# Performance work log

Hardware: AMD Instinct MI355X
Metric: run time of the kernel (lower is better)

## Reference

```python
import jax, jax.numpy as jnp
import numpy as np

K = 3
LAMBDA_AMP = 0.1
N_NODES = 100000
N_EDGES = 1600000
D_FEAT = 50


def _proximal_l21(x, lambda_):
    # rowwise L2,1 shrinkage: scale each row by max(||row||-lambda,0)/||row||
    row_norm = jnp.linalg.norm(x, axis=1)  # [N]
    score = jnp.maximum(row_norm - lambda_, 0.0)
    score = jnp.where(row_norm > 0, score / jnp.where(row_norm > 0, row_norm, 1.0), score)
    return score[:, None] * x


def setup_inputs() -> dict:
    key = jax.random.key(0)
    k1, k2, k3, k4 = jax.random.split(key, 4)
    feat = jax.random.normal(k1, (N_NODES, D_FEAT), dtype=jnp.float32)
    edge_weight = jax.random.uniform(k2, (N_EDGES,), dtype=jnp.float32)
    src = jax.random.randint(k3, (N_EDGES,), 0, N_NODES, dtype=jnp.int32)
    dst = jax.random.randint(k4, (N_EDGES,), 0, N_NODES, dtype=jnp.int32)
    return {"feat": feat, "edge_weight": edge_weight, "src": src, "dst": dst}


def reference(feat, edge_weight, src, dst):
    n = feat.shape[0]
    # add self-loops (add_self_loop=True), self-loop weight = 1
    loop = jnp.arange(n, dtype=src.dtype)
    src_f = jnp.concatenate([src, loop])
    dst_f = jnp.concatenate([dst, loop])
    ew = jnp.concatenate([edge_weight, jnp.ones((n,), dtype=edge_weight.dtype)])

    # norm='both': w_ji = ew / (sqrt(out_deg(j)) * sqrt(in_deg(i))), weighted degrees
    out_deg = jax.ops.segment_sum(ew, src_f, num_segments=n)
    in_deg = jax.ops.segment_sum(ew, dst_f, num_segments=n)
    inv_sqrt_out = jnp.where(out_deg > 0, out_deg, 1.0) ** -0.5 * (out_deg > 0)
    inv_sqrt_in = jnp.where(in_deg > 0, in_deg, 1.0) ** -0.5 * (in_deg > 0)
    w = ew * inv_sqrt_out[src_f] * inv_sqrt_in[dst_f]  # [E+N]

    lam = LAMBDA_AMP
    gamma = 1.0 / (2.0 * (1.0 - lam))
    hh = feat
    x = feat
    for _ in range(K):
        # compute_LX: x - A_norm x  (u_mul_e + sum == SpMM over edges)
        agg = jax.ops.segment_sum(x[src_f] * w[:, None], dst_f, num_segments=n)
        lx = x - agg
        y = x - gamma * 2.0 * (1.0 - lam) * lx
        x = hh + _proximal_l21(y - hh, gamma * lam)
    return x
```

## Files before the change

### kernel.cpp

```cpp
#include <hip/hip_runtime.h>
#include <hip/hip_bf16.h>
#include <hip/hip_fp16.h>

#define D 50
#define PADH 64
#define GLAM 0.05555555555555555f
#define SCAN_B 1024
#define FIXS 8388608.0f
#define INV_FIXS (1.0f / 8388608.0f)
#define WSC 32768.0f
#define INV_WSC (1.0f / 32768.0f)
#define EPB 4096
#define EPT 8
#define B2T 512
#define BSH 9
#define BMSK 511u
#define BT 512
#define MAXB 256
#define MAXRUN 12288
#define NXCD 8

typedef unsigned long long u64;

__global__ void k_b1p(const int* __restrict__ src, const int* __restrict__ dst,
                      int* __restrict__ mat, const float* __restrict__ feat,
                      __half* __restrict__ xp, int e, int nblk, int nbuk, int n) {
    if ((int)blockIdx.x < nblk) {
        __shared__ unsigned hd[MAXB], hs[MAXB];
        for (int j = threadIdx.x; j < nbuk; j += blockDim.x) { hd[j] = 0; hs[j] = 0; }
        __syncthreads();
        int base = blockIdx.x * EPB;
        int end = base + EPB; if (end > e) end = e;
        for (int i = base + threadIdx.x; i < end; i += blockDim.x) {
            int t = __builtin_nontemporal_load(dst + i);
            int s = __builtin_nontemporal_load(src + i);
            atomicAdd(&hd[t >> BSH], 1u);
            atomicAdd(&hs[s >> BSH], 1u);
        }
        __syncthreads();
        for (int j = threadIdx.x; j < nbuk; j += blockDim.x) {
            mat[j * nblk + blockIdx.x] = (int)hd[j];
            mat[(nbuk + j) * nblk + blockIdx.x] = (int)hs[j];
        }
    } else {
        int i = ((int)blockIdx.x - nblk) * (int)blockDim.x + (int)threadIdx.x;
        if (i < n * PADH) {
            int node = i >> 6, col = i & 63;
            xp[i] = (col < D) ? __float2half_rn(feat[node * D + col]) : __half(0.0f);
        }
    }
}

__global__ void k_scan1(const int* __restrict__ cnt, int* __restrict__ out,
                        int* __restrict__ bsum, int n) {
    __shared__ int s[SCAN_B];
    int i = blockIdx.x * SCAN_B + threadIdx.x;
    int v = (i < n) ? cnt[i] : 0;
    s[threadIdx.x] = v; __syncthreads();
    for (int off = 1; off < SCAN_B; off <<= 1) {
        int t = (threadIdx.x >= (unsigned)off) ? s[threadIdx.x - off] : 0;
        __syncthreads();
        s[threadIdx.x] += t; __syncthreads();
    }
    if (i < n) out[i] = s[threadIdx.x] - v;
    if (threadIdx.x == SCAN_B - 1) bsum[blockIdx.x] = s[threadIdx.x];
}

__global__ void k_scan2(int* __restrict__ bsum, int nb) {
    __shared__ int s[SCAN_B];
    int v = (threadIdx.x < (unsigned)nb) ? bsum[threadIdx.x] : 0;
    s[threadIdx.x] = v; __syncthreads();
    for (int off = 1; off < SCAN_B; off <<= 1) {
        int t = (threadIdx.x >= (unsigned)off) ? s[threadIdx.x - off] : 0;
        __syncthreads();
        s[threadIdx.x] += t; __syncthreads();
    }
    if (threadIdx.x < (unsigned)nb) bsum[threadIdx.x] = s[threadIdx.x] - v;
}

__global__ void k_scan3(int* __restrict__ out, const int* __restrict__ bsum, int n) {
    int i = blockIdx.x * SCAN_B + threadIdx.x;
    if (i < n) out[i] += bsum[blockIdx.x];
}

__device__ __forceinline__ int xcd_swz(int p, int nwg) {
    int q = nwg / NXCD, r = nwg % NXCD;
    int xcd = p % NXCD, idx = p / NXCD;
    return (xcd < r ? xcd * (q + 1) : r * (q + 1) + (xcd - r) * q) + idx;
}

__global__ __launch_bounds__(B2T, 4) void k_b2(
                     const float* __restrict__ ew, const int* __restrict__ src,
                     const int* __restrict__ dst, const int* __restrict__ msc,
                     u64* __restrict__ bind, unsigned* __restrict__ bins,
                     int e, int nblk, int nbuk) {
    __shared__ unsigned cd[MAXB], cs[MAXB];
    __shared__ unsigned ld[MAXB], ls[MAXB];
    __shared__ int gbd[MAXB], gbs[MAXB];
    __shared__ u64 sd[EPB];
    __shared__ unsigned ss[EPB];
    __shared__ unsigned char bdd[EPB], bds[EPB];
    int tid = threadIdx.x;
    int wb = xcd_swz((int)blockIdx.x, nblk);
    if (tid < MAXB) { cd[tid] = 0; cs[tid] = 0; }
    __syncthreads();
    int base = wb * EPB;
    int end = base + EPB; if (end > e) end = e;
    int m = end - base;

    int sv[EPT], tv[EPT]; float wv[EPT];
    #pragma unroll
    for (int k = 0; k < EPT; ++k) {
        int i = base + k * B2T + tid;
        bool ok = (i < end);
        sv[k] = ok ? __builtin_nontemporal_load(src + i) : 0;
        tv[k] = ok ? __builtin_nontemporal_load(dst + i) : 0;
        wv[k] = ok ? __builtin_nontemporal_load(ew + i) : 0.0f;
        if (ok) {
            atomicAdd(&cd[(unsigned)tv[k] >> BSH], 1u);
            atomicAdd(&cs[(unsigned)sv[k] >> BSH], 1u);
        }
    }
    __syncthreads();

    unsigned vd = 0, vs = 0;
    if (tid < MAXB) { vd = cd[tid]; vs = cs[tid]; ld[tid] = vd; ls[tid] = vs; }
    __syncthreads();
    for (int off = 1; off < MAXB; off <<= 1) {
        unsigned td = 0, ts = 0;
        if (tid < MAXB && tid >= off) { td = ld[tid - off]; ts = ls[tid - off]; }
        __syncthreads();
        if (tid < MAXB) { ld[tid] += td; ls[tid] += ts; }
        __syncthreads();
    }
    if (tid < MAXB) {
        ld[tid] -= vd; ls[tid] -= vs;
        cd[tid] = ld[tid]; cs[tid] = ls[tid];
        if (tid < nbuk) {
            gbd[tid] = msc[tid * nblk + wb];
            gbs[tid] = msc[(nbuk + tid) * nblk + wb] - e;
        }
    }
    __syncthreads();

    #pragma unroll
    for (int k = 0; k < EPT; ++k) {
        int i = base + k * B2T + tid;
        if (i < end) {
            float w = wv[k]; int s = sv[k]; int t = tv[k];
            unsigned wfix = (unsigned)(w * FIXS + 0.5f);
            if (wfix > 0x7FFFFFu) wfix = 0x7FFFFFu;
            unsigned tb = (unsigned)t >> BSH, sb = (unsigned)s >> BSH;
            unsigned pd = atomicAdd(&cd[tb], 1u);
            sd[pd] = ((u64)__float_as_uint(w) << 32)
                   | ((unsigned)s << BSH) | (unsigned)(t & BMSK);
            bdd[pd] = (unsigned char)tb;
            unsigned ps = atomicAdd(&cs[sb], 1u);
            ss[ps] = (wfix << BSH) | (unsigned)(s & BMSK);
            bds[ps] = (unsigned char)sb;
        }
    }
    __syncthreads();

    for (int p = tid; p < m; p += blockDim.x) {
        unsigned jd = bdd[p];
        bind[gbd[jd] + (int)(p - ld[jd])] = sd[p];
        unsigned js = bds[p];
        bins[gbs[js] + (int)(p - ls[js])] = ss[p];
    }
}

__global__ void k_srcdeg(const unsigned* __restrict__ bins, const int* __restrict__ msc,
                         float* __restrict__ iso, int n, int nblk, int nbuk, int e) {
    __shared__ unsigned wl[BT];
    wl[threadIdx.x] = 0;
    __syncthreads();
    int b = blockIdx.x;
    int start = msc[(nbuk + b) * nblk] - e;
    int end = (b + 1 < nbuk) ? (msc[(nbuk + b + 1) * nblk] - e) : e;
    for (int i = start + threadIdx.x; i < end; i += blockDim.x) {
        unsigned r = bins[i];
        atomicAdd(&wl[r & BMSK], r >> BSH);
    }
    __syncthreads();
    int node = b * BT + threadIdx.x;
    if (node < n)
        iso[node] = rsqrtf(1.0f + (float)wl[threadIdx.x] * INV_FIXS);
}

__global__ void k_dstfill(const u64* __restrict__ bind, const int* __restrict__ msc,
                          const float* __restrict__ iso, float* __restrict__ isi,
                          int* __restrict__ cnt, int* __restrict__ rowptr,
                          unsigned* __restrict__ pe, int n, int nblk, int nbuk, int e) {
    __shared__ unsigned pst[MAXRUN];
    __shared__ unsigned cl[BT], wl[BT], cur[BT];
    __shared__ int sc[BT];
    __shared__ float isL[BT];
    cl[threadIdx.x] = 0; wl[threadIdx.x] = 0;
    __syncthreads();
    int b = blockIdx.x;
    int start = msc[b * nblk];
    int end = (b + 1 < nbuk) ? msc[(b + 1) * nblk] : e;
    int run = end - start;
    bool fast = (run <= MAXRUN);

    for (int i = start + threadIdx.x; i < end; i += blockDim.x) {
        u64 r = bind[i];
        unsigned loc = (unsigned)r & BMSK;
        float w = __uint_as_float((unsigned)(r >> 32));
        unsigned wfix = (unsigned)(w * FIXS + 0.5f);
        if (wfix > 0x7FFFFFu) wfix = 0x7FFFFFu;
        atomicAdd(&cl[loc], 1u);
        atomicAdd(&wl[loc], wfix);
    }
    __syncthreads();

    int myc = (int)cl[threadIdx.x];
    sc[threadIdx.x] = myc;
    __syncthreads();
    for (int off = 1; off < BT; off <<= 1) {
        int t = (threadIdx.x >= (unsigned)off) ? sc[threadIdx.x - off] : 0;
        __syncthreads();
        sc[threadIdx.x] += t;
        __syncthreads();
    }
    int lex = sc[threadIdx.x] - myc;
    int lrp = start + lex;

    float myisi = rsqrtf(1.0f + (float)wl[threadIdx.x] * INV_FIXS);
    isL[threadIdx.x] = myisi;
    cur[threadIdx.x] = fast ? (unsigned)lex : (unsigned)lrp;

    int node = b * BT + threadIdx.x;
    if (node < n) {
        isi[node] = myisi;
        cnt[node] = myc;
        rowptr[node] = lrp;
    }
    __syncthreads();

    if (fast) {
        for (int i = start + threadIdx.x; i < end; i += blockDim.x) {
            u64 r = bind[i];
            unsigned lo = (unsigned)r;
            unsigned tloc = lo & BMSK;
            unsigned s = lo >> BSH;
            float w = __uint_as_float((unsigned)(r >> 32));
            float wv = w * iso[s] * isL[tloc];
            unsigned wq = (unsigned)(wv * WSC + 0.5f);
            if (wq > 32767u) wq = 32767u;
            unsigned pos = atomicAdd(&cur[tloc], 1u);
            pst[pos] = (s << 15) | wq;
        }
        __syncthreads();
        for (int p = threadIdx.x; p < run; p += blockDim.x)
            pe[start + p] = pst[p];
    } else {
        for (int i = start + threadIdx.x; i < end; i += blockDim.x) {
            u64 r = bind[i];
            unsigned lo = (unsigned)r;
            unsigned tloc = lo & BMSK;
            unsigned s = lo >> BSH;
            float w = __uint_as_float((unsigned)(r >> 32));
            float wv = w * iso[s] * isL[tloc];
            unsigned wq = (unsigned)(wv * WSC + 0.5f);
            if (wq > 32767u) wq = 32767u;
            unsigned pos = atomicAdd(&cur[tloc], 1u);
            pe[pos] = (s << 15) | wq;
        }
    }
}

__device__ __forceinline__ void acc_edge(const uint4& u, float w,
                                         float& a0, float& a1, float& a2, float& a3,
                                         float& a4, float& a5, float& a6, float& a7) {
    const __half2* hp = (const __half2*)&u;
    float2 f0 = __half22float2(hp[0]);
    float2 f1 = __half22float2(hp[1]);
    float2 f2 = __half22float2(hp[2]);
    float2 f3 = __half22float2(hp[3]);
    a0 = fmaf(w, f0.x, a0); a1 = fmaf(w, f0.y, a1);
    a2 = fmaf(w, f1.x, a2); a3 = fmaf(w, f1.y, a3);
    a4 = fmaf(w, f2.x, a4); a5 = fmaf(w, f2.y, a5);
    a6 = fmaf(w, f3.x, a6); a7 = fmaf(w, f3.y, a7);
}

__global__ void k_iter(const int* __restrict__ rowptr, const int* __restrict__ cnt,
                       const unsigned* __restrict__ pe, const __half* __restrict__ xin,
                       const __half* __restrict__ xpF, const float* __restrict__ iso,
                       const float* __restrict__ isi, __half* __restrict__ hout,
                       float* __restrict__ fout, int n, int final_iter) {
    int lane = threadIdx.x & 63;
    int c    = lane & 7;
    int waveId = (blockIdx.x * blockDim.x + threadIdx.x) >> 6;
    int node = waveId * 8 + (lane >> 3);
    if (node >= n) return;

    float a0 = 0.f, a1 = 0.f, a2 = 0.f, a3 = 0.f;
    float a4 = 0.f, a5 = 0.f, a6 = 0.f, a7 = 0.f;

    int beg = rowptr[node], m = cnt[node];

    int j = 0;
    for (; j + 8 <= m; j += 8) {
        unsigned p0 = pe[beg + j];
        unsigned p1 = pe[beg + j + 1];
        unsigned p2 = pe[beg + j + 2];
        unsigned p3 = pe[beg + j + 3];
        unsigned p4 = pe[beg + j + 4];
        unsigned p5 = pe[beg + j + 5];
        unsigned p6 = pe[beg + j + 6];
        unsigned p7 = pe[beg + j + 7];
        unsigned s0 = p0 >> 15; float w0 = (float)(p0 & 32767u) * INV_WSC;
        unsigned s1 = p1 >> 15; float w1 = (float)(p1 & 32767u) * INV_WSC;
        unsigned s2 = p2 >> 15; float w2 = (float)(p2 & 32767u) * INV_WSC;
        unsigned s3 = p3 >> 15; float w3 = (float)(p3 & 32767u) * INV_WSC;
        unsigned s4 = p4 >> 15; float w4 = (float)(p4 & 32767u) * INV_WSC;
        unsigned s5 = p5 >> 15; float w5 = (float)(p5 & 32767u) * INV_WSC;
        unsigned s6 = p6 >> 15; float w6 = (float)(p6 & 32767u) * INV_WSC;
        unsigned s7 = p7 >> 15; float w7 = (float)(p7 & 32767u) * INV_WSC;
        uint4 u0 = *(const uint4*)(xin + ((size_t)s0 << 6) + (c << 3));
        uint4 u1 = *(const uint4*)(xin + ((size_t)s1 << 6) + (c << 3));
        uint4 u2 = *(const uint4*)(xin + ((size_t)s2 << 6) + (c << 3));
        uint4 u3 = *(const uint4*)(xin + ((size_t)s3 << 6) + (c << 3));
        uint4 u4 = *(const uint4*)(xin + ((size_t)s4 << 6) + (c << 3));
        uint4 u5 = *(const uint4*)(xin + ((size_t)s5 << 6) + (c << 3));
        uint4 u6 = *(const uint4*)(xin + ((size_t)s6 << 6) + (c << 3));
        uint4 u7 = *(const uint4*)(xin + ((size_t)s7 << 6) + (c << 3));
        acc_edge(u0, w0, a0, a1, a2, a3, a4, a5, a6, a7);
        acc_edge(u1, w1, a0, a1, a2, a3, a4, a5, a6, a7);
        acc_edge(u2, w2, a0, a1, a2, a3, a4, a5, a6, a7);
        acc_edge(u3, w3, a0, a1, a2, a3, a4, a5, a6, a7);
        acc_edge(u4, w4, a0, a1, a2, a3, a4, a5, a6, a7);
        acc_edge(u5, w5, a0, a1, a2, a3, a4, a5, a6, a7);
        acc_edge(u6, w6, a0, a1, a2, a3, a4, a5, a6, a7);
        acc_edge(u7, w7, a0, a1, a2, a3, a4, a5, a6, a7);
    }
    for (; j + 4 <= m; j += 4) {
        unsigned p0 = pe[beg + j];
        unsigned p1 = pe[beg + j + 1];
        unsigned p2 = pe[beg + j + 2];
        unsigned p3 = pe[beg + j + 3];
        unsigned s0 = p0 >> 15; float w0 = (float)(p0 & 32767u) * INV_WSC;
        unsigned s1 = p1 >> 15; float w1 = (float)(p1 & 32767u) * INV_WSC;
        unsigned s2 = p2 >> 15; float w2 = (float)(p2 & 32767u) * INV_WSC;
        unsigned s3 = p3 >> 15; float w3 = (float)(p3 & 32767u) * INV_WSC;
        uint4 u0 = *(const uint4*)(xin + ((size_t)s0 << 6) + (c << 3));
        uint4 u1 = *(const uint4*)(xin + ((size_t)s1 << 6) + (c << 3));
        uint4 u2 = *(const uint4*)(xin + ((size_t)s2 << 6) + (c << 3));
        uint4 u3 = *(const uint4*)(xin + ((size_t)s3 << 6) + (c << 3));
        acc_edge(u0, w0, a0, a1, a2, a3, a4, a5, a6, a7);
        acc_edge(u1, w1, a0, a1, a2, a3, a4, a5, a6, a7);
        acc_edge(u2, w2, a0, a1, a2, a3, a4, a5, a6, a7);
        acc_edge(u3, w3, a0, a1, a2, a3, a4, a5, a6, a7);
    }
    for (; j < m; ++j) {
        unsigned p0 = pe[beg + j];
        unsigned s0 = p0 >> 15;
        float    w0 = (float)(p0 & 32767u) * INV_WSC;
        uint4 u0 = *(const uint4*)(xin + ((size_t)s0 << 6) + (c << 3));
        acc_edge(u0, w0, a0, a1, a2, a3, a4, a5, a6, a7);
    }

    float selfw = iso[node] * isi[node];
    {
        uint4 u = *(const uint4*)(xin + ((size_t)node << 6) + (c << 3));
        acc_edge(u, selfw, a0, a1, a2, a3, a4, a5, a6, a7);
    }

    float f[8];
    {
        uint4 u = *(const uint4*)(xpF + ((size_t)node << 6) + (c << 3));
        const __half2* hp = (const __half2*)&u;
        float2 f0 = __half22float2(hp[0]);
        float2 f1 = __half22float2(hp[1]);
        float2 f2 = __half22float2(hp[2]);
        float2 f3 = __half22float2(hp[3]);
        f[0] = f0.x; f[1] = f0.y; f[2] = f1.x; f[3] = f1.y;
        f[4] = f2.x; f[5] = f2.y; f[6] = f3.x; f[7] = f3.y;
    }

    float d0 = a0 - f[0], d1 = a1 - f[1], d2 = a2 - f[2], d3 = a3 - f[3];
    float d4 = a4 - f[4], d5 = a5 - f[5], d6 = a6 - f[6], d7 = a7 - f[7];

    float ssum = d0*d0 + d1*d1 + d2*d2 + d3*d3 + d4*d4 + d5*d5 + d6*d6 + d7*d7;
    ssum += __shfl_xor(ssum, 1, 64);
    ssum += __shfl_xor(ssum, 2, 64);
    ssum += __shfl_xor(ssum, 4, 64);
    float norm = sqrtf(ssum);
    float sc = (norm > 0.0f) ? fmaxf(norm - GLAM, 0.0f) / norm : 0.0f;

    float o0 = f[0] + sc * d0, o1 = f[1] + sc * d1;
    float o2 = f[2] + sc * d2, o3 = f[3] + sc * d3;
    float o4 = f[4] + sc * d4, o5 = f[5] + sc * d5;
    float o6 = f[6] + sc * d6, o7 = f[7] + sc * d7;
    if (!final_iter) {
        __half2 h0 = __float22half2_rn(make_float2(o0, o1));
        __half2 h1 = __float22half2_rn(make_float2(o2, o3));
        __half2 h2 = __float22half2_rn(make_float2(o4, o5));
        __half2 h3 = __float22half2_rn(make_float2(o6, o7));
        uint4 u;
        u.x = *(unsigned*)&h0; u.y = *(unsigned*)&h1;
        u.z = *(unsigned*)&h2; u.w = *(unsigned*)&h3;
        *(uint4*)(hout + ((size_t)node << 6) + (c << 3)) = u;
    } else {
        float o[8] = {o0, o1, o2, o3, o4, o5, o6, o7};
        int fb = c << 3;
        #pragma unroll
        for (int k = 0; k < 4; ++k) {
            int ff = fb + (k << 1);
            if (ff + 1 < D) {
                float2 v; v.x = o[k * 2]; v.y = o[k * 2 + 1];
                *(float2*)(fout + (size_t)node * D + ff) = v;
            }
        }
    }
}

extern "C" void kernel_launch(void* const* d_in, const int* in_sizes, int n_in,
                              void* d_out, int out_size, void* d_ws, size_t ws_size,
                              hipStream_t stream) {
    const float* feat = (const float*)d_in[0];
    const float* ew   = (const float*)d_in[1];
    const int* src = (const int*)d_in[2];
    const int* dst = (const int*)d_in[3];

    const int nd = in_sizes[0];
    const int n  = nd / D;
    const int e  = in_sizes[1];
    const int np = n * PADH;

    const int nbuk = (n + BT - 1) / BT;
    const int nblk = (e + EPB - 1) / EPB;
    const int nm   = 2 * nbuk * nblk;

    __half*   xpF    = (__half*)d_ws;
    __half*   xpA    = xpF + np;
    __half*   xpB    = xpA + np;
    u64*      bind   = (u64*)(xpB + np);
    unsigned* pe     = (unsigned*)(bind + e);
    unsigned* bins   = pe + e;
    int*      mat    = (int*)(bins + e);
    int*      msc    = mat + nm;
    float*    isi    = (float*)(msc + nm);
    float*    iso    = isi + n;
    int*      cnt    = (int*)(iso + n);
    int*      rowptr = cnt + n;
    int*      bsum   = rowptr + n;
    float*    out    = (float*)d_out;

    const int B = 256;
    const int gP  = (np + B2T - 1) / B2T;
    const int NBm = (nm + SCAN_B - 1) / SCAN_B;

    k_b1p<<<nblk + gP, B2T, 0, stream>>>(src, dst, mat, feat, xpF, e, nblk, nbuk, n);
    k_scan1<<<NBm, SCAN_B, 0, stream>>>(mat, msc, bsum, nm);
    k_scan2<<<1, SCAN_B, 0, stream>>>(bsum, NBm);
    k_scan3<<<NBm, SCAN_B, 0, stream>>>(msc, bsum, nm);
    k_b2<<<nblk, B2T, 0, stream>>>(ew, src, dst, msc, bind, bins, e, nblk, nbuk);
    k_srcdeg<<<nbuk, BT, 0, stream>>>(bins, msc, iso, n, nblk, nbuk, e);
    k_dstfill<<<nbuk, BT, 0, stream>>>(bind, msc, iso, isi, cnt, rowptr, pe, n, nblk, nbuk, e);

    const int nodesPerBlock = (B / 64) * 8;
    const int iterGrid = (n + nodesPerBlock - 1) / nodesPerBlock;

    k_iter<<<iterGrid, B, 0, stream>>>(rowptr, cnt, pe, xpF, xpF, iso, isi, xpA, out, n, 0);
    k_iter<<<iterGrid, B, 0, stream>>>(rowptr, cnt, pe, xpA, xpF, iso, isi, xpB, out, n, 0);
    k_iter<<<iterGrid, B, 0, stream>>>(rowptr, cnt, pe, xpB, xpF, iso, isi, xpA, out, n, 1);
}
```

Baseline: 237.5 us.

## Factor degree normalization out of edge weights and fuse degree kernels

Per-edge weights now store only the raw edge weight. The source-degree scaling is folded into the stored features (x * iso) and the destination scaling is applied once per node after aggregation. This lets the src-degree and dst-fill kernels run concurrently as two halves of one launch, removing the dependency of dst-fill on iso. The separate scan3 kernel is also dropped by adding block sums at read time. Quantizing raw weights and pre-scaled features in fp16 may change rounding behaviour, and the half-split blocks may be imbalanced.

After: 242.4 us. 2.0% more time.

```diff
diff --git a/kernel.cpp b/kernel.cpp
--- a/kernel.cpp
+++ b/kernel.cpp
@@ -78,11 +78,6 @@
     if (threadIdx.x < (unsigned)nb) bsum[threadIdx.x] = s[threadIdx.x] - v;
 }
 
-__global__ void k_scan3(int* __restrict__ out, const int* __restrict__ bsum, int n) {
-    int i = blockIdx.x * SCAN_B + threadIdx.x;
-    if (i < n) out[i] += bsum[blockIdx.x];
-}
-
 __device__ __forceinline__ int xcd_swz(int p, int nwg) {
     int q = nwg / NXCD, r = nwg % NXCD;
     int xcd = p % NXCD, idx = p / NXCD;
@@ -92,6 +87,7 @@
 __global__ __launch_bounds__(B2T, 4) void k_b2(
                      const float* __restrict__ ew, const int* __restrict__ src,
                      const int* __restrict__ dst, const int* __restrict__ msc,
+                     const int* __restrict__ bsum,
                      u64* __restrict__ bind, unsigned* __restrict__ bins,
                      int e, int nblk, int nbuk) {
     __shared__ unsigned cd[MAXB], cs[MAXB];
@@ -137,8 +133,10 @@
         ld[tid] -= vd; ls[tid] -= vs;
         cd[tid] = ld[tid]; cs[tid] = ls[tid];
         if (tid < nbuk) {
-            gbd[tid] = msc[tid * nblk + wb];
-            gbs[tid] = msc[(nbuk + tid) * nblk + wb] - e;
+            int id1 = tid * nblk + wb;
+            int id2 = (nbuk + tid) * nblk + wb;
+            gbd[tid] = msc[id1] + bsum[id1 >> 10];
+            gbs[tid] = msc[id2] + bsum[id2 >> 10] - e;
         }
     }
     __syncthreads();
@@ -170,103 +168,120 @@
     }
 }
 
-__global__ void k_srcdeg(const unsigned* __restrict__ bins, const int* __restrict__ msc,
-                         float* __restrict__ iso, int n, int nblk, int nbuk, int e) {
-    __shared__ unsigned wl[BT];
-    wl[threadIdx.x] = 0;
-    __syncthreads();
-    int b = blockIdx.x;
-    int start = msc[(nbuk + b) * nblk] - e;
-    int end = (b + 1 < nbuk) ? (msc[(nbuk + b + 1) * nblk] - e) : e;
-    for (int i = start + threadIdx.x; i < end; i += blockDim.x) {
-        unsigned r = bins[i];
-        atomicAdd(&wl[r & BMSK], r >> BSH);
-    }
-    __syncthreads();
-    int node = b * BT + threadIdx.x;
-    if (node < n)
-        iso[node] = rsqrtf(1.0f + (float)wl[threadIdx.x] * INV_FIXS);
-}
-
-__global__ void k_dstfill(const u64* __restrict__ bind, const int* __restrict__ msc,
-                          const float* __restrict__ iso, float* __restrict__ isi,
-                          int* __restrict__ cnt, int* __restrict__ rowptr,
-                          unsigned* __restrict__ pe, int n, int nblk, int nbuk, int e) {
+__global__ void k_deg(const u64* __restrict__ bind, const unsigned* __restrict__ bins,
+                      const int* __restrict__ msc, const int* __restrict__ bsum,
+                      const float* __restrict__ feat, float* __restrict__ iso,
+                      float* __restrict__ isi, int* __restrict__ cnt,
+                      int* __restrict__ rowptr, unsigned* __restrict__ pe,
+                      __half* __restrict__ xq, int n, int nblk, int nbuk, int e) {
     __shared__ unsigned pst[MAXRUN];
     __shared__ unsigned cl[BT], wl[BT], cur[BT];
     __shared__ int sc[BT];
-    __shared__ float isL[BT];
-    cl[threadIdx.x] = 0; wl[threadIdx.x] = 0;
-    __syncthreads();
-    int b = blockIdx.x;
-    int start = msc[b * nblk];
-    int end = (b + 1 < nbuk) ? msc[(b + 1) * nblk] : e;
-    int run = end - start;
-    bool fast = (run <= MAXRUN);
-
-    for (int i = start + threadIdx.x; i < end; i += blockDim.x) {
-        u64 r = bind[i];
-        unsigned loc = (unsigned)r & BMSK;
-        float w = __uint_as_float((unsigned)(r >> 32));
-        unsigned wfix = (unsigned)(w * FIXS + 0.5f);
-        if (wfix > 0x7FFFFFu) wfix = 0x7FFFFFu;
-        atomicAdd(&cl[loc], 1u);
-        atomicAdd(&wl[loc], wfix);
-    }
-    __syncthreads();
-
-    int myc = (int)cl[threadIdx.x];
-    sc[threadIdx.x] = myc;
-    __syncthreads();
-    for (int off = 1; off < BT; off <<= 1) {
-        int t = (threadIdx.x >= (unsigned)off) ? sc[threadIdx.x - off] : 0;
-        __syncthreads();
-        sc[threadIdx.x] += t;
-        __syncthreads();
-    }
-    int lex = sc[threadIdx.x] - myc;
-    int lrp = start + lex;
-
-    float myisi = rsqrtf(1.0f + (float)wl[threadIdx.x] * INV_FIXS);
-    isL[threadIdx.x] = myisi;
-    cur[threadIdx.x] = fast ? (unsigned)lex : (unsigned)lrp;
-
-    int node = b * BT + threadIdx.x;
-    if (node < n) {
-        isi[node] = myisi;
-        cnt[node] = myc;
-        rowptr[node] = lrp;
-    }
-    __syncthreads();
-
-    if (fast) {
-        for (int i = start + threadIdx.x; i < end; i += blockDim.x) {
+    __shared__ float fl[BT];
+    int half = (int)blockIdx.x & 1;
+    int b    = (int)blockIdx.x >> 1;
+    int tid  = threadIdx.x;
+
+    if (half) {
+        wl[tid] = 0;
+        __syncthreads();
+        int id1 = (nbuk + b) * nblk;
+        int start = msc[id1] + bsum[id1 >> 10] - e;
+        int end;
+        if (b + 1 < nbuk) {
+            int id2 = (nbuk + b + 1) * nblk;
+            end = msc[id2] + bsum[id2 >> 10] - e;
+        } else end = e;
+        for (int i = start + tid; i < end; i += blockDim.x) {
+            unsigned r = bins[i];
+            atomicAdd(&wl[r & BMSK], r >> BSH);
+        }
+        __syncthreads();
+        int node = b * BT + tid;
+        float v = rsqrtf(1.0f + (float)wl[tid] * INV_FIXS);
+        fl[tid] = v;
+        if (node < n) iso[node] = v;
+        __syncthreads();
+        int base = b * BT;
+        for (int idx = tid; idx < BT * PADH; idx += BT) {
+            int ln = idx >> 6, col = idx & 63;
+            int nd2 = base + ln;
+            if (nd2 < n)
+                xq[((size_t)nd2 << 6) + col] = (col < D)
+                    ? __float2half_rn(feat[nd2 * D + col] * fl[ln])
+                    : __half(0.0f);
+        }
+    } else {
+        cl[tid] = 0; wl[tid] = 0;
+        __syncthreads();
+        int id1 = b * nblk;
+        int start = msc[id1] + bsum[id1 >> 10];
+        int id2 = (b + 1) * nblk;
+        int end = msc[id2] + bsum[id2 >> 10];
+        int run = end - start;
+        bool fast = (run <= MAXRUN);
+
+        for (int i = start + tid; i < end; i += blockDim.x) {
             u64 r = bind[i];
-            unsigned lo = (unsigned)r;
-            unsigned tloc = lo & BMSK;
-            unsigned s = lo >> BSH;
+            unsigned loc = (unsigned)r & BMSK;
             float w = __uint_as_float((unsigned)(r >> 32));
-            float wv = w * iso[s] * isL[tloc];
-            unsigned wq = (unsigned)(wv * WSC + 0.5f);
-            if (wq > 32767u) wq = 32767u;
-            unsigned pos = atomicAdd(&cur[tloc], 1u);
-            pst[pos] = (s << 15) | wq;
-        }
-        __syncthreads();
-        for (int p = threadIdx.x; p < run; p += blockDim.x)
-            pe[start + p] = pst[p];
-    } else {
-        for (int i = start + threadIdx.x; i < end; i += blockDim.x) {
-            u64 r = bind[i];
-            unsigned lo = (unsigned)r;
-            unsigned tloc = lo & BMSK;
-            unsigned s = lo >> BSH;
-            float w = __uint_as_float((unsigned)(r >> 32));
-            float wv = w * iso[s] * isL[tloc];
-            unsigned wq = (unsigned)(wv * WSC + 0.5f);
-            if (wq > 32767u) wq = 32767u;
-            unsigned pos = atomicAdd(&cur[tloc], 1u);
-            pe[pos] = (s << 15) | wq;
+            unsigned wfix = (unsigned)(w * FIXS + 0.5f);
+            if (wfix > 0x7FFFFFu) wfix = 0x7FFFFFu;
+            atomicAdd(&cl[loc], 1u);
+            atomicAdd(&wl[loc], wfix);
+        }
+        __syncthreads();
+
+        int myc = (int)cl[tid];
+        sc[tid] = myc;
+        __syncthreads();
+        for (int off = 1; off < BT; off <<= 1) {
+            int t = (tid >= off) ? sc[tid - off] : 0;
+            __syncthreads();
+            sc[tid] += t;
+            __syncthreads();
+        }
+        int lex = sc[tid] - myc;
+        int lrp = start + lex;
+
+        float myisi = rsqrtf(1.0f + (float)wl[tid] * INV_FIXS);
+        cur[tid] = fast ? (unsigned)lex : (unsigned)lrp;
+
+        int node = b * BT + tid;
+        if (node < n) {
+            isi[node] = myisi;
+            cnt[node] = myc;
+            rowptr[node] = lrp;
+        }
+        __syncthreads();
+
+        if (fast) {
+            for (int i = start + tid; i < end; i += blockDim.x) {
+                u64 r = bind[i];
+                unsigned lo = (unsigned)r;
+                unsigned tloc = lo & BMSK;
+                unsigned s = lo >> BSH;
+                float w = __uint_as_float((unsigned)(r >> 32));
+                unsigned wq = (unsigned)(w * WSC + 0.5f);
+                if (wq > 32767u) wq = 32767u;
+                unsigned pos = atomicAdd(&cur[tloc], 1u);
+                pst[pos] = (s << 15) | wq;
+            }
+            __syncthreads();
+            for (int p = tid; p < run; p += blockDim.x)
+                pe[start + p] = pst[p];
+        } else {
+            for (int i = start + tid; i < end; i += blockDim.x) {
+                u64 r = bind[i];
+                unsigned lo = (unsigned)r;
+                unsigned tloc = lo & BMSK;
+                unsigned s = lo >> BSH;
+                float w = __uint_as_float((unsigned)(r >> 32));
+                unsigned wq = (unsigned)(w * WSC + 0.5f);
+                if (wq > 32767u) wq = 32767u;
+                unsigned pos = atomicAdd(&cur[tloc], 1u);
+                pe[pos] = (s << 15) | wq;
+            }
         }
     }
 }
@@ -362,11 +377,14 @@
         acc_edge(u0, w0, a0, a1, a2, a3, a4, a5, a6, a7);
     }
 
-    float selfw = iso[node] * isi[node];
     {
         uint4 u = *(const uint4*)(xin + ((size_t)node << 6) + (c << 3));
-        acc_edge(u, selfw, a0, a1, a2, a3, a4, a5, a6, a7);
-    }
+        acc_edge(u, 1.0f, a0, a1, a2, a3, a4, a5, a6, a7);
+    }
+
+    float si = isi[node];
+    a0 *= si; a1 *= si; a2 *= si; a3 *= si;
+    a4 *= si; a5 *= si; a6 *= si; a7 *= si;
 
     float f[8];
     {
@@ -395,10 +413,11 @@
     float o4 = f[4] + sc * d4, o5 = f[5] + sc * d5;
     float o6 = f[6] + sc * d6, o7 = f[7] + sc * d7;
     if (!final_iter) {
-        __half2 h0 = __float22half2_rn(make_float2(o0, o1));
-        __half2 h1 = __float22half2_rn(make_float2(o2, o3));
-        __half2 h2 = __float22half2_rn(make_float2(o4, o5));
-        __half2 h3 = __float22half2_rn(make_float2(o6, o7));
+        float so = iso[node];
+        __half2 h0 = __float22half2_rn(make_float2(so * o0, so * o1));
+        __half2 h1 = __float22half2_rn(make_float2(so * o2, so * o3));
+        __half2 h2 = __float22half2_rn(make_float2(so * o4, so * o5));
+        __half2 h3 = __float22half2_rn(make_float2(so * o6, so * o7));
         uint4 u;
         u.x = *(unsigned*)&h0; u.y = *(unsigned*)&h1;
         u.z = *(unsigned*)&h2; u.w = *(unsigned*)&h3;
@@ -456,15 +475,14 @@
     k_b1p<<<nblk + gP, B2T, 0, stream>>>(src, dst, mat, feat, xpF, e, nblk, nbuk, n);
     k_scan1<<<NBm, SCAN_B, 0, stream>>>(mat, msc, bsum, nm);
     k_scan2<<<1, SCAN_B, 0, stream>>>(bsum, NBm);
-    k_scan3<<<NBm, SCAN_B, 0, stream>>>(msc, bsum, nm);
-    k_b2<<<nblk, B2T, 0, stream>>>(ew, src, dst, msc, bind, bins, e, nblk, nbuk);
-    k_srcdeg<<<nbuk, BT, 0, stream>>>(bins, msc, iso, n, nblk, nbuk, e);
-    k_dstfill<<<nbuk, BT, 0, stream>>>(bind, msc, iso, isi, cnt, rowptr, pe, n, nblk, nbuk, e);
+    k_b2<<<nblk, B2T, 0, stream>>>(ew, src, dst, msc, bsum, bind, bins, e, nblk, nbuk);
+    k_deg<<<2 * nbuk, BT, 0, stream>>>(bind, bins, msc, bsum, feat, iso, isi,
+                                       cnt, rowptr, pe, xpB, n, nblk, nbuk, e);
 
     const int nodesPerBlock = (B / 64) * 8;
     const int iterGrid = (n + nodesPerBlock - 1) / nodesPerBlock;
 
-    k_iter<<<iterGrid, B, 0, stream>>>(rowptr, cnt, pe, xpF, xpF, iso, isi, xpA, out, n, 0);
+    k_iter<<<iterGrid, B, 0, stream>>>(rowptr, cnt, pe, xpB, xpF, iso, isi, xpA, out, n, 0);
     k_iter<<<iterGrid, B, 0, stream>>>(rowptr, cnt, pe, xpA, xpF, iso, isi, xpB, out, n, 0);
     k_iter<<<iterGrid, B, 0, stream>>>(rowptr, cnt, pe, xpB, xpF, iso, isi, xpA, out, n, 1);
 }
```
